# Performance work log

Measured on AMD Instinct MI355X. Metric: run time of the kernel, lower is better.

Reference implementation:

```python
import jax, jax.numpy as jnp
import numpy as np

B, H, W = 8, 64, 64
DIM1, DIM2 = 384, 256
NH, DH = 8, 32
INNER = NH * DH
EPS = 1e-5


def _layernorm(x, w, b):
    mu = jnp.mean(x, axis=-1, keepdims=True)
    var = jnp.mean((x - mu) ** 2, axis=-1, keepdims=True)
    return (x - mu) * jax.lax.rsqrt(var + EPS) * w + b


def _axial_attn(q, k, v, scale):
    # q,k,v: [B,H,W,nh,dh]; row attention over H, col attention over W
    sh = jnp.einsum('biwnd,bjwnd->bwnij', q, k) * scale  # [B,W,nh,H,H]
    oh = jnp.einsum('bwnij,bjwnd->biwnd', jax.nn.softmax(sh, axis=-1), v)
    sw = jnp.einsum('bhind,bhjnd->bhnij', q, k) * scale  # [B,H,nh,W,W]
    ow = jnp.einsum('bhnij,bhjnd->bhind', jax.nn.softmax(sw, axis=-1), v)
    return oh + ow  # [B,H,W,nh,dh]


def setup_inputs() -> dict:
    key = jax.random.key(0)
    ks = jax.random.split(key, 16)
    s1 = 1.0 / np.sqrt(DIM1)
    s2 = 1.0 / np.sqrt(DIM2)
    si = 1.0 / np.sqrt(INNER)
    return {
        'x1': jax.random.normal(ks[0], (B, DIM1, H, W), jnp.float32),
        'x2': jax.random.normal(ks[1], (B, DIM2, H, W), jnp.float32),
        'ln1q_w': jnp.ones((DIM1,), jnp.float32),
        'ln1q_b': jnp.zeros((DIM1,), jnp.float32),
        'ln2kv_w': jnp.ones((DIM2,), jnp.float32),
        'ln2kv_b': jnp.zeros((DIM2,), jnp.float32),
        'Wq1': jax.random.normal(ks[2], (DIM1, INNER), jnp.float32) * s1,
        'Wkv2': jax.random.normal(ks[3], (DIM2, 2 * INNER), jnp.float32) * s2,
        'Wout1': jax.random.normal(ks[4], (INNER, DIM2), jnp.float32) * si,
        'bout1': jnp.zeros((DIM2,), jnp.float32),
        'ln2q_w': jnp.ones((DIM2,), jnp.float32),
        'ln2q_b': jnp.zeros((DIM2,), jnp.float32),
        'ln1kv_w': jnp.ones((DIM1,), jnp.float32),
        'ln1kv_b': jnp.zeros((DIM1,), jnp.float32),
        'Wq2': jax.random.normal(ks[5], (DIM2, INNER), jnp.float32) * s2,
        'Wkv1': jax.random.normal(ks[6], (DIM1, 2 * INNER), jnp.float32) * s1,
        'Wout2': jax.random.normal(ks[7], (INNER, DIM2), jnp.float32) * si,
        'bout2': jnp.zeros((DIM2,), jnp.float32),
        'Wsc': jax.random.normal(ks[8], (DIM2, DIM1), jnp.float32) * s1,  # 1x1 conv [out,in]
        'bn_gamma': jnp.ones((DIM2,), jnp.float32),
        'bn_beta': jnp.zeros((DIM2,), jnp.float32),
        'bn_mean': jnp.zeros((DIM2,), jnp.float32),
        'bn_var': jnp.ones((DIM2,), jnp.float32),
    }


def reference(x1, x2, ln1q_w, ln1q_b, ln2kv_w, ln2kv_b, Wq1, Wkv2, Wout1, bout1,
              ln2q_w, ln2q_b, ln1kv_w, ln1kv_b, Wq2, Wkv1, Wout2, bout2,
              Wsc, bn_gamma, bn_beta, bn_mean, bn_var):
    b, c1, h, w = x1.shape
    scale = DH ** -0.5
    x1f = jnp.transpose(x1, (0, 2, 3, 1))  # [B,H,W,C1]
    x2f = jnp.transpose(x2, (0, 2, 3, 1))  # [B,H,W,C2]

    def heads(t):
        return t.reshape(b, h, w, NH, DH)

    # branch 1: q from x1, kv from x2
    q1 = _layernorm(x1f, ln1q_w, ln1q_b) @ Wq1
    kv2 = _layernorm(x2f, ln2kv_w, ln2kv_b) @ Wkv2
    k2, v2 = jnp.split(kv2, 2, axis=-1)
    o1 = _axial_attn(heads(q1), heads(k2), heads(v2), scale)
    fused1 = o1.reshape(b, h, w, INNER) @ Wout1 + bout1
    # shortcut: 1x1 conv + BN (inference stats)
    sc = jnp.einsum('bhwc,oc->bhwo', x1f, Wsc)
    sc = (sc - bn_mean) * jax.lax.rsqrt(bn_var + EPS) * bn_gamma + bn_beta
    y1 = sc + fused1

    # branch 2: q from x2, kv from x1
    q2 = _layernorm(x2f, ln2q_w, ln2q_b) @ Wq2
    kv1 = _layernorm(x1f, ln1kv_w, ln1kv_b) @ Wkv1
    k1, v1 = jnp.split(kv1, 2, axis=-1)
    o2 = _axial_attn(heads(q2), heads(k1), heads(v1), scale)
    fused2 = o2.reshape(b, h, w, INNER) @ Wout2 + bout2
    y2 = x2f + fused2

    out = y1 + y2  # [B,H,W,C2]
    return jnp.transpose(out, (0, 3, 1, 2))
```

## Files before the change

### kernel.cpp

```cpp
#include <hip/hip_runtime.h>

typedef unsigned short u16;
typedef unsigned int u32;
typedef float v4f __attribute__((ext_vector_type(4)));
typedef __bf16 v8bf __attribute__((ext_vector_type(8)));

__device__ __forceinline__ float bf2f(u16 v) {
  union { u32 u; float f; } x; x.u = ((u32)v) << 16; return x.f;
}
__device__ __forceinline__ u16 f2bf(float f) {
  union { float f; u32 u; } x; x.f = f;
  u32 u = x.u;
  return (u16)((u + 0x7FFFu + ((u >> 16) & 1u)) >> 16);
}
__device__ __forceinline__ u32 f2u(float f) {
  union { float f; u32 u; } x; x.f = f; return x.u;
}
__device__ __forceinline__ u32 pk2bf(float a, float b) {
  const u32 au = f2u(a) + 0x8000u;
  const u32 bu = f2u(b) + 0x8000u;
  return (bu & 0xFFFF0000u) | (au >> 16);
}

struct Ptrs { const void* p[23]; };

__global__ __launch_bounds__(256) void convert_all(Ptrs ps, u16* __restrict__ cx1,
                                                   u16* __restrict__ cx2,
                                                   u16* __restrict__ cw) {
  static const int sz[23]  = {12582912, 8388608, 384, 384, 256, 256, 98304, 131072,
                              65536, 256, 256, 256, 384, 384, 65536, 196608, 65536,
                              256, 98304, 256, 256, 256, 256};
  static const int off[23] = {0, 0, 0, 384, 768, 1024, 1280, 99584, 230656, 296192,
                              296448, 296704, 296960, 297344, 297728, 363264, 559872,
                              625408, 625664, 723968, 724224, 724480, 724736};
  const int ti = blockIdx.y;
  const int n8 = sz[ti] >> 3;
  const bool isf32 = (((const u32*)ps.p[2])[0] == 0x3F800000u);
  u16* dst = (ti == 0) ? cx1 : (ti == 1) ? cx2 : (cw + off[ti]);
  const void* src = ps.p[ti];
  const int stride = gridDim.x * blockDim.x;
  for (int i = blockIdx.x * blockDim.x + threadIdx.x; i < n8; i += stride) {
    if (isf32) {
      const float4 f0 = ((const float4*)src)[2*i];
      const float4 f1 = ((const float4*)src)[2*i + 1];
      u16 tmp[8];
      tmp[0] = f2bf(f0.x); tmp[1] = f2bf(f0.y); tmp[2] = f2bf(f0.z); tmp[3] = f2bf(f0.w);
      tmp[4] = f2bf(f1.x); tmp[5] = f2bf(f1.y); tmp[6] = f2bf(f1.z); tmp[7] = f2bf(f1.w);
      ((uint4*)dst)[i] = *(const uint4*)tmp;
    } else {
      ((uint4*)dst)[i] = ((const uint4*)src)[i];
    }
  }
}

__global__ void prep_bt(const u16* __restrict__ lnq_w, const u16* __restrict__ lnq_b,
                        const u16* __restrict__ lnkv_w, const u16* __restrict__ lnkv_b,
                        const u16* __restrict__ Wq, const u16* __restrict__ Wkv,
                        u16* __restrict__ BT, float* __restrict__ bias) {
  const int C = blockDim.x;
  const int j = blockIdx.x;
  const int c = threadIdx.x;
  float w, bco, wv;
  if (j < 256) { w = bf2f(lnq_w[c]); bco = bf2f(lnq_b[c]); wv = bf2f(Wq[c*256 + j]); }
  else         { w = bf2f(lnkv_w[c]); bco = bf2f(lnkv_b[c]); wv = bf2f(Wkv[c*512 + (j-256)]); }
  BT[(size_t)j*C + c] = f2bf(w * wv);
  __shared__ float red[384];
  red[c] = bco * wv;
  __syncthreads();
  if (c == 0) { float s = 0.f; for (int i = 0; i < C; i++) s += red[i]; bias[j] = s; }
}

__global__ void prep_fin(const u16* __restrict__ Wout1, const u16* __restrict__ Wout2,
                         const u16* __restrict__ Wsc, const u16* __restrict__ bout1,
                         const u16* __restrict__ bout2, const u16* __restrict__ gam,
                         const u16* __restrict__ bet, const u16* __restrict__ mean,
                         const u16* __restrict__ var, u16* __restrict__ BT,
                         float* __restrict__ bias) {
  const int o = blockIdx.x, t = threadIdx.x;
  const float g = rsqrtf(bf2f(var[o]) + 1e-5f) * bf2f(gam[o]);
  for (int idx = t; idx < 1408; idx += 256) {
    float v;
    if (idx < 512)       v = bf2f(Wout1[(idx & 255)*256 + o]);
    else if (idx < 1024) v = bf2f(Wout2[((idx - 512) & 255)*256 + o]);
    else                 v = bf2f(Wsc[o*384 + (idx - 1024)]) * g;
    BT[(size_t)o*1408 + idx] = f2bf(v);
  }
  if (t == 0) bias[o] = bf2f(bet[o]) - bf2f(mean[o])*g + bf2f(bout1[o]) + bf2f(bout2[o]);
}

__global__ __launch_bounds__(256) void ln_c384(const u16* __restrict__ x,
                                               u16* __restrict__ xn, u16* __restrict__ xraw) {
  __shared__ u16 tile[384*66];
  __shared__ float rsum[4][64], rsq[4][64], smean[64], srstd[64];
  const int t = threadIdx.x, w = t & 63, g = t >> 6;
  const int bh = blockIdx.x, b = bh >> 6, h = bh & 63;
  const u16* src = x + (size_t)b*384*4096 + h*64 + w;
  float sum = 0.f, sq = 0.f;
  for (int j = 0; j < 96; j++) {
    const int c = g*96 + j;
    const u16 uv = src[(size_t)c*4096];
    tile[c*66 + w] = uv;
    const float v = bf2f(uv); sum += v; sq += v*v;
  }
  rsum[g][w] = sum; rsq[g][w] = sq;
  __syncthreads();
  if (t < 64) {
    const float s = rsum[0][t]+rsum[1][t]+rsum[2][t]+rsum[3][t];
    const float q = rsq[0][t]+rsq[1][t]+rsq[2][t]+rsq[3][t];
    const float mean = s * (1.0f/384.0f);
    float var = q * (1.0f/384.0f) - mean*mean;
    if (var < 0.f) var = 0.f;
    smean[t] = mean; srstd[t] = rsqrtf(var + 1e-5f);
  }
  __syncthreads();
  const size_t pos0 = (size_t)bh * 64;
  for (int i = 0; i < 96; i++) {
    const int flat = i*256 + t;
    const int ww = flat / 384, c = flat - ww*384;
    const u16 uv = tile[c*66 + ww];
    const float v = (bf2f(uv) - smean[ww]) * srstd[ww];
    const size_t p = pos0 + ww;
    xn[p*384 + c] = f2bf(v);
    xraw[p*384 + c] = uv;
  }
}

__global__ __launch_bounds__(256) void ln_c256(const u16* __restrict__ x,
                                               u16* __restrict__ xn) {
  __shared__ u16 tile[256*66];
  __shared__ float rsum[4][64], rsq[4][64], smean[64], srstd[64];
  const int t = threadIdx.x, w = t & 63, g = t >> 6;
  const int bh = blockIdx.x, b = bh >> 6, h = bh & 63;
  const u16* src = x + (size_t)b*256*4096 + h*64 + w;
  float sum = 0.f, sq = 0.f;
  for (int j = 0; j < 64; j++) {
    const int c = g*64 + j;
    const u16 uv = src[(size_t)c*4096];
    tile[c*66 + w] = uv;
    const float v = bf2f(uv); sum += v; sq += v*v;
  }
  rsum[g][w] = sum; rsq[g][w] = sq;
  __syncthreads();
  if (t < 64) {
    const float s = rsum[0][t]+rsum[1][t]+rsum[2][t]+rsum[3][t];
    const float q = rsq[0][t]+rsq[1][t]+rsq[2][t]+rsq[3][t];
    const float mean = s * (1.0f/256.0f);
    float var = q * (1.0f/256.0f) - mean*mean;
    if (var < 0.f) var = 0.f;
    smean[t] = mean; srstd[t] = rsqrtf(var + 1e-5f);
  }
  __syncthreads();
  const size_t pos0 = (size_t)bh * 64;
  for (int i = 0; i < 64; i++) {
    const int flat = i*256 + t;
    const int ww = flat >> 8, c = flat & 255;
    const float v = (bf2f(tile[c*66 + ww]) - smean[ww]) * srstd[ww];
    xn[(pos0 + ww)*256 + c] = f2bf(v);
  }
}

__global__ __launch_bounds__(256) void gemm_bt(const u16* __restrict__ A,
                                               const u16* __restrict__ BT,
                                               u16* __restrict__ C,
                                               const float* __restrict__ bias,
                                               int N, int K) {
  __shared__ u16 lsA[128*40];
  __shared__ u16 lsB[128*40];
  const int t = threadIdx.x;
  const int m0 = blockIdx.x * 128, n0 = blockIdx.y * 128;
  const int lane = t & 63, wv = t >> 6;
  const int wm = wv & 1, wn = wv >> 1;
  const int lo = lane & 15, hi = lane >> 4;
  const int r0 = t >> 2, c8 = (t & 3) << 3;
  const u16* Ab = A + (size_t)(m0 + r0) * K + c8;
  const u16* Bb = BT + (size_t)(n0 + r0) * K + c8;
  v4f acc[4][4] = {};
  for (int kb = 0; kb < K; kb += 32) {
    uint4 a0 = *(const uint4*)(Ab + kb);
    uint4 a1 = *(const uint4*)(Ab + (size_t)64*K + kb);
    uint4 b0 = *(const uint4*)(Bb + kb);
    uint4 b1 = *(const uint4*)(Bb + (size_t)64*K + kb);
    __syncthreads();
    *(uint4*)&lsA[r0*40 + c8] = a0;
    *(uint4*)&lsA[(r0+64)*40 + c8] = a1;
    *(uint4*)&lsB[r0*40 + c8] = b0;
    *(uint4*)&lsB[(r0+64)*40 + c8] = b1;
    __syncthreads();
    v8bf av[4], bv[4];
#pragma unroll
    for (int i = 0; i < 4; i++) av[i] = *(const v8bf*)&lsA[(wm*64 + i*16 + lo)*40 + hi*8];
#pragma unroll
    for (int i = 0; i < 4; i++) bv[i] = *(const v8bf*)&lsB[(wn*64 + i*16 + lo)*40 + hi*8];
#pragma unroll
    for (int mt = 0; mt < 4; mt++)
#pragma unroll
      for (int nt = 0; nt < 4; nt++)
        acc[mt][nt] = __builtin_amdgcn_mfma_f32_16x16x32_bf16(av[mt], bv[nt], acc[mt][nt], 0, 0, 0);
  }
#pragma unroll
  for (int mt = 0; mt < 4; mt++) {
    const int row = m0 + wm*64 + mt*16 + hi*4;
#pragma unroll
    for (int nt = 0; nt < 4; nt++) {
      const int col = n0 + wn*64 + nt*16 + lo;
      const float bs = bias[col];
#pragma unroll
      for (int r = 0; r < 4; r++)
        C[(size_t)(row + r) * N + col] = f2bf(acc[mt][nt][r] + bs);
    }
  }
}

__global__ __launch_bounds__(256) void gemm_final(const u16* __restrict__ Ao,
                                                  const u16* __restrict__ Ar,
                                                  const u16* __restrict__ BT,
                                                  const float* __restrict__ bias,
                                                  const u16* __restrict__ x2c,
                                                  const u32* __restrict__ probe,
                                                  void* __restrict__ outv) {
  __shared__ u16 smem[16640];
  u16* lsA = smem;
  u16* lsB = smem + 5120;
  const int t = threadIdx.x;
  const int m0 = blockIdx.x * 128, n0 = blockIdx.y * 128;
  const int lane = t & 63, wv = t >> 6;
  const int wm = wv & 1, wn = wv >> 1;
  const int lo = lane & 15, hi = lane >> 4;
  const int r0 = t >> 2, c8 = (t & 3) << 3;
  const u16* ArR = Ar + (size_t)(m0 + r0) * 384 + c8;
  const u16* Bb  = BT + (size_t)(n0 + r0) * 1408 + c8;
  v4f acc[4][4] = {};
  for (int kb = 0; kb < 1408; kb += 32) {
    uint4 a0, a1;
    if (kb < 1024) {
      const u16* ap = Ao + ((size_t)(kb >> 5) * 32768 + m0 + r0) * 32 + c8;
      a0 = *(const uint4*)ap;
      a1 = *(const uint4*)(ap + 64*32);
    } else {
      a0 = *(const uint4*)(ArR + (kb-1024));
      a1 = *(const uint4*)(ArR + 64*384 + (kb-1024));
    }
    uint4 b0 = *(const uint4*)(Bb + kb);
    uint4 b1 = *(const uint4*)(Bb + 64*1408 + kb);
    __syncthreads();
    *(uint4*)&lsA[r0*40 + c8] = a0;
    *(uint4*)&lsA[(r0+64)*40 + c8] = a1;
    *(uint4*)&lsB[r0*40 + c8] = b0;
    *(uint4*)&lsB[(r0+64)*40 + c8] = b1;
    __syncthreads();
    v8bf av[4], bv[4];
#pragma unroll
    for (int i = 0; i < 4; i++) av[i] = *(const v8bf*)&lsA[(wm*64 + i*16 + lo)*40 + hi*8];
#pragma unroll
    for (int i = 0; i < 4; i++) bv[i] = *(const v8bf*)&lsB[(wn*64 + i*16 + lo)*40 + hi*8];
#pragma unroll
    for (int mt = 0; mt < 4; mt++)
#pragma unroll
      for (int nt = 0; nt < 4; nt++)
        acc[mt][nt] = __builtin_amdgcn_mfma_f32_16x16x32_bf16(av[mt], bv[nt], acc[mt][nt], 0, 0, 0);
  }
  __syncthreads();
#pragma unroll
  for (int mt = 0; mt < 4; mt++)
#pragma unroll
    for (int nt = 0; nt < 4; nt++) {
      const int nl = wn*64 + nt*16 + lo;
      const float bs = bias[n0 + nl];
#pragma unroll
      for (int r = 0; r < 4; r++)
        smem[(wm*64 + mt*16 + hi*4 + r)*130 + nl] = f2bf(acc[mt][nt][r] + bs);
    }
  __syncthreads();
  const bool isf32 = (probe[0] == 0x3F800000u);
  const int bh0 = blockIdx.x * 2;
  for (int i = 0; i < 64; i++) {
    const int flat = i*256 + t;
    const int nl = flat >> 7;
    const int rem = flat & 127;
    const int mb = rem >> 6, w = rem & 63;
    const int bh = bh0 + mb, b = bh >> 6, h = bh & 63;
    const size_t oidx = ((size_t)(b*256 + n0 + nl)*64 + h)*64 + w;
    const float val = bf2f(smem[(mb*64 + w)*130 + nl]) + bf2f(x2c[oidx]);
    if (isf32) ((float*)outv)[oidx] = val;
    else       ((u16*)outv)[oidx]   = f2bf(val);
  }
}

__global__ __launch_bounds__(512) void attn(const u16* __restrict__ qkv1,
                                            const u16* __restrict__ qkv2,
                                            u16* __restrict__ Ao) {
  __shared__ __attribute__((aligned(16))) u16 smem[8 * 2560];
  const int t = threadIdx.x;
  const int head = t >> 6, lane = t & 63;
  const int lo = lane & 15, quad = lane >> 4;
  u16* sw = smem + head * 2560;
  const int bx = blockIdx.x;
  const int z = blockIdx.y;
  const int br = z >> 1, dir = z & 1;
  const int b = bx >> 6, x = bx & 63;
  const u16* Qb  = (br == 0) ? qkv1 : qkv2;
  const u16* KVb = (br == 0) ? qkv2 : qkv1;
  const int qc = head*32, kc = 256 + head*32, vc = 512 + head*32;
  const int pbase = (dir == 0) ? (b*4096 + x) : ((b*64 + x)*64);
  const int pstr  = (dir == 0) ? 64 : 1;

  {
    const u16* vr = KVb + (size_t)(pbase + lane*pstr)*768 + vc;
    u16 vbuf[32];
#pragma unroll
    for (int i = 0; i < 4; i++) *(uint4*)&vbuf[i*8] = *(const uint4*)(vr + i*8);
    const int khi = lane >> 3, klo = lane & 7;
#pragma unroll
    for (int d = 0; d < 32; d++)
      sw[d*64 + ((khi ^ (d & 7)) << 3) + klo] = vbuf[d];
  }
  __syncthreads();

  v8bf qa[4], ka[4];
#pragma unroll
  for (int i = 0; i < 4; i++) {
    const size_t p = (size_t)(pbase + (i*16 + lo)*pstr) * 768;
    qa[i] = *(const v8bf*)(Qb + p + qc + quad*8);
    ka[i] = *(const v8bf*)(KVb + p + kc + quad*8);
  }

  v4f s[4][4];
#pragma unroll
  for (int qt = 0; qt < 4; qt++)
#pragma unroll
    for (int kt = 0; kt < 4; kt++) {
      v4f z4 = {};
      s[qt][kt] = __builtin_amdgcn_mfma_f32_16x16x32_bf16(ka[kt], qa[qt], z4, 0, 0, 0);
    }

  v8bf va[2][2];
#pragma unroll
  for (int mt = 0; mt < 2; mt++)
#pragma unroll
    for (int ks = 0; ks < 2; ks++) {
      const int d = mt*16 + lo;
      va[mt][ks] = *(const v8bf*)&sw[d*64 + (((ks*4 + quad) ^ (d & 7)) << 3)];
    }

  const float scale = 0.17677669529663687f;
  v4f o[2][4] = {};
#pragma unroll
  for (int qt = 0; qt < 4; qt++) {
    float tv[16];
    float mx = -1e30f;
#pragma unroll
    for (int kt = 0; kt < 4; kt++)
#pragma unroll
      for (int r = 0; r < 4; r++) {
        const float v = s[qt][kt][r] * scale;
        tv[kt*4 + r] = v;
        mx = fmaxf(mx, v);
      }
    mx = fmaxf(mx, __shfl_xor(mx, 16));
    mx = fmaxf(mx, __shfl_xor(mx, 32));
    float sm = 0.f;
#pragma unroll
    for (int i = 0; i < 16; i++) { tv[i] = __expf(tv[i] - mx); sm += tv[i]; }
    sm += __shfl_xor(sm, 16);
    sm += __shfl_xor(sm, 32);
    const float inv = 1.0f / sm;
    u32 pk[4][2];
#pragma unroll
    for (int kt = 0; kt < 4; kt++)
#pragma unroll
      for (int rp = 0; rp < 2; rp++)
        pk[kt][rp] = pk2bf(tv[kt*4 + rp*2] * inv, tv[kt*4 + rp*2 + 1] * inv);
    u32 pw[2][4];
#pragma unroll
    for (int ks = 0; ks < 2; ks++)
#pragma unroll
      for (int rp = 0; rp < 2; rp++) {
        const u32 v16 = (quad < 2)  ? pk[2*ks][rp]   : pk[2*ks+1][rp];
        const u32 v32 = (quad < 2)  ? pk[2*ks+1][rp] : pk[2*ks][rp];
        const u32 v48 = (quad & 1)  ? pk[2*ks+1][rp] : pk[2*ks][rp];
        const u32 r16 = (u32)__shfl_xor((int)v16, 16);
        const u32 r32 = (u32)__shfl_xor((int)v32, 32);
        const u32 r48 = (u32)__shfl_xor((int)v48, 48);
        const u32 wlo = (quad == 0) ? pk[2*ks][rp] : (quad == 1) ? r48 : (quad == 2) ? r32 : r16;
        const u32 whi = (quad == 0) ? r16 : (quad == 1) ? r32 : (quad == 2) ? r48 : pk[2*ks+1][rp];
        pw[ks][rp] = wlo;
        pw[ks][2 + rp] = whi;
      }
#pragma unroll
    for (int ks = 0; ks < 2; ks++) {
      union { u32 u[4]; v8bf v; } pb;
      pb.u[0] = pw[ks][0]; pb.u[1] = pw[ks][1]; pb.u[2] = pw[ks][2]; pb.u[3] = pw[ks][3];
#pragma unroll
      for (int mt = 0; mt < 2; mt++)
        o[mt][qt] = __builtin_amdgcn_mfma_f32_16x16x32_bf16(va[mt][ks], pb.v, o[mt][qt], 0, 0, 0);
    }
  }

  __syncthreads();
#pragma unroll
  for (int mt = 0; mt < 2; mt++)
#pragma unroll
    for (int nt = 0; nt < 4; nt++)
#pragma unroll
      for (int rp = 0; rp < 2; rp++) {
        const u32 pkv = pk2bf(o[mt][nt][rp*2], o[mt][nt][rp*2 + 1]);
        *(u32*)&sw[(nt*16 + lo)*40 + mt*16 + quad*4 + rp*2] = pkv;
      }
  __syncthreads();
  {
    const size_t sbase = (size_t)(z*8 + head) * 32768 + pbase;
#pragma unroll
    for (int it = 0; it < 4; it++) {
      const int chunk = it*64 + lane;
      const int row = chunk >> 2, ic = chunk & 3;
      *(uint4*)&Ao[(sbase + (size_t)row*pstr)*32 + ic*8] = *(const uint4*)&sw[row*40 + ic*8];
    }
  }
}

extern "C" void kernel_launch(void* const* d_in, const int* in_sizes, int n_in,
                              void* d_out, int out_size, void* d_ws, size_t ws_size,
                              hipStream_t stream) {
  char* ws = (char*)d_ws;
  u16* Ao    = (u16*)(ws);
  u16* Araw  = (u16*)(ws + 67108864);
  u16* qkv1  = (u16*)(ws + 92274688);
  u16* qkv2  = (u16*)(ws + 142606336);
  u16* cx2   = (u16*)(ws + 192937984);
  u16* cw    = (u16*)(ws + 209715200);
  u16* BT1   = (u16*)(ws + 211165184);
  u16* BT2   = (u16*)(ws + 211755008);
  u16* BTf   = (u16*)(ws + 212148224);
  float* bias1 = (float*)(ws + 212869120);
  float* bias2 = (float*)(ws + 212872192);
  float* biasf = (float*)(ws + 212875264);
  u16* cx1 = qkv1;
  u16* x1n = Ao;
  u16* x2n = Ao + 12582912;

  u16* c_ln1q_w = cw + 0,     *c_ln1q_b = cw + 384;
  u16* c_ln2kv_w = cw + 768,  *c_ln2kv_b = cw + 1024;
  u16* c_Wq1 = cw + 1280,     *c_Wkv2 = cw + 99584;
  u16* c_Wout1 = cw + 230656, *c_bout1 = cw + 296192;
  u16* c_ln2q_w = cw + 296448,*c_ln2q_b = cw + 296704;
  u16* c_ln1kv_w = cw + 296960,*c_ln1kv_b = cw + 297344;
  u16* c_Wq2 = cw + 297728,   *c_Wkv1 = cw + 363264;
  u16* c_Wout2 = cw + 559872, *c_bout2 = cw + 625408;
  u16* c_Wsc = cw + 625664;
  u16* c_bn_g = cw + 723968,  *c_bn_b = cw + 724224;
  u16* c_bn_m = cw + 724480,  *c_bn_v = cw + 724736;

  Ptrs ps;
  for (int i = 0; i < 23; i++) ps.p[i] = d_in[i];

  convert_all<<<dim3(512, 23), 256, 0, stream>>>(ps, cx1, cx2, cw);
  prep_bt<<<768, 384, 0, stream>>>(c_ln1q_w, c_ln1q_b, c_ln1kv_w, c_ln1kv_b, c_Wq1, c_Wkv1, BT1, bias1);
  prep_bt<<<768, 256, 0, stream>>>(c_ln2q_w, c_ln2q_b, c_ln2kv_w, c_ln2kv_b, c_Wq2, c_Wkv2, BT2, bias2);
  prep_fin<<<256, 256, 0, stream>>>(c_Wout1, c_Wout2, c_Wsc, c_bout1, c_bout2,
                                    c_bn_g, c_bn_b, c_bn_m, c_bn_v, BTf, biasf);
  ln_c384<<<512, 256, 0, stream>>>(cx1, x1n, Araw);
  ln_c256<<<512, 256, 0, stream>>>(cx2, x2n);
  gemm_bt<<<dim3(256, 6), 256, 0, stream>>>(x1n, BT1, qkv1, bias1, 768, 384);
  gemm_bt<<<dim3(256, 6), 256, 0, stream>>>(x2n, BT2, qkv2, bias2, 768, 256);
  attn<<<dim3(512, 4), 512, 0, stream>>>(qkv1, qkv2, Ao);
  gemm_final<<<dim3(256, 2), 256, 0, stream>>>(Ao, Araw, BTf, biasf, cx2,
                                               (const u32*)d_in[2], d_out);
}
```

Baseline: 371.1 us.

## Prefetch next K-tile into registers in GEMMs; widen final GEMM to 512 threads

```diff
diff --git a/kernel.cpp b/kernel.cpp
--- a/kernel.cpp
+++ b/kernel.cpp
@@ -174,18 +174,24 @@
   const int r0 = t >> 2, c8 = (t & 3) << 3;
   const u16* Ab = A + (size_t)(m0 + r0) * K + c8;
   const u16* Bb = BT + (size_t)(n0 + r0) * K + c8;
+  uint4 a0 = *(const uint4*)(Ab);
+  uint4 a1 = *(const uint4*)(Ab + (size_t)64*K);
+  uint4 b0 = *(const uint4*)(Bb);
+  uint4 b1 = *(const uint4*)(Bb + (size_t)64*K);
   v4f acc[4][4] = {};
   for (int kb = 0; kb < K; kb += 32) {
-    uint4 a0 = *(const uint4*)(Ab + kb);
-    uint4 a1 = *(const uint4*)(Ab + (size_t)64*K + kb);
-    uint4 b0 = *(const uint4*)(Bb + kb);
-    uint4 b1 = *(const uint4*)(Bb + (size_t)64*K + kb);
     __syncthreads();
     *(uint4*)&lsA[r0*40 + c8] = a0;
     *(uint4*)&lsA[(r0+64)*40 + c8] = a1;
     *(uint4*)&lsB[r0*40 + c8] = b0;
     *(uint4*)&lsB[(r0+64)*40 + c8] = b1;
     __syncthreads();
+    if (kb + 32 < K) {
+      a0 = *(const uint4*)(Ab + kb + 32);
+      a1 = *(const uint4*)(Ab + (size_t)64*K + kb + 32);
+      b0 = *(const uint4*)(Bb + kb + 32);
+      b1 = *(const uint4*)(Bb + (size_t)64*K + kb + 32);
+    }
     v8bf av[4], bv[4];
 #pragma unroll
     for (int i = 0; i < 4; i++) av[i] = *(const v8bf*)&lsA[(wm*64 + i*16 + lo)*40 + hi*8];
@@ -211,7 +217,7 @@
   }
 }
 
-__global__ __launch_bounds__(256) void gemm_final(const u16* __restrict__ Ao,
+__global__ __launch_bounds__(512) void gemm_final(const u16* __restrict__ Ao,
                                                   const u16* __restrict__ Ar,
                                                   const u16* __restrict__ BT,
                                                   const float* __restrict__ bias,
@@ -224,57 +230,56 @@
   const int t = threadIdx.x;
   const int m0 = blockIdx.x * 128, n0 = blockIdx.y * 128;
   const int lane = t & 63, wv = t >> 6;
-  const int wm = wv & 1, wn = wv >> 1;
+  const int wm = wv >> 1, wn = wv & 1;
   const int lo = lane & 15, hi = lane >> 4;
   const int r0 = t >> 2, c8 = (t & 3) << 3;
   const u16* ArR = Ar + (size_t)(m0 + r0) * 384 + c8;
   const u16* Bb  = BT + (size_t)(n0 + r0) * 1408 + c8;
-  v4f acc[4][4] = {};
+
+  uint4 a, bq;
+  {
+    a = *(const uint4*)(Ao + ((size_t)(0) * 32768 + m0 + r0) * 32 + c8);
+    bq = *(const uint4*)(Bb);
+  }
+  v4f acc[2][4] = {};
   for (int kb = 0; kb < 1408; kb += 32) {
-    uint4 a0, a1;
-    if (kb < 1024) {
-      const u16* ap = Ao + ((size_t)(kb >> 5) * 32768 + m0 + r0) * 32 + c8;
-      a0 = *(const uint4*)ap;
-      a1 = *(const uint4*)(ap + 64*32);
-    } else {
-      a0 = *(const uint4*)(ArR + (kb-1024));
-      a1 = *(const uint4*)(ArR + 64*384 + (kb-1024));
-    }
-    uint4 b0 = *(const uint4*)(Bb + kb);
-    uint4 b1 = *(const uint4*)(Bb + 64*1408 + kb);
     __syncthreads();
-    *(uint4*)&lsA[r0*40 + c8] = a0;
-    *(uint4*)&lsA[(r0+64)*40 + c8] = a1;
-    *(uint4*)&lsB[r0*40 + c8] = b0;
-    *(uint4*)&lsB[(r0+64)*40 + c8] = b1;
+    *(uint4*)&lsA[r0*40 + c8] = a;
+    *(uint4*)&lsB[r0*40 + c8] = bq;
     __syncthreads();
-    v8bf av[4], bv[4];
-#pragma unroll
-    for (int i = 0; i < 4; i++) av[i] = *(const v8bf*)&lsA[(wm*64 + i*16 + lo)*40 + hi*8];
+    const int kn = kb + 32;
+    if (kn < 1408) {
+      if (kn < 1024) a = *(const uint4*)(Ao + ((size_t)(kn >> 5) * 32768 + m0 + r0) * 32 + c8);
+      else           a = *(const uint4*)(ArR + (kn - 1024));
+      bq = *(const uint4*)(Bb + kn);
+    }
+    v8bf av[2], bv[4];
+#pragma unroll
+    for (int i = 0; i < 2; i++) av[i] = *(const v8bf*)&lsA[(wm*32 + i*16 + lo)*40 + hi*8];
 #pragma unroll
     for (int i = 0; i < 4; i++) bv[i] = *(const v8bf*)&lsB[(wn*64 + i*16 + lo)*40 + hi*8];
 #pragma unroll
-    for (int mt = 0; mt < 4; mt++)
+    for (int mt = 0; mt < 2; mt++)
 #pragma unroll
       for (int nt = 0; nt < 4; nt++)
         acc[mt][nt] = __builtin_amdgcn_mfma_f32_16x16x32_bf16(av[mt], bv[nt], acc[mt][nt], 0, 0, 0);
   }
   __syncthreads();
 #pragma unroll
-  for (int mt = 0; mt < 4; mt++)
+  for (int mt = 0; mt < 2; mt++)
 #pragma unroll
     for (int nt = 0; nt < 4; nt++) {
       const int nl = wn*64 + nt*16 + lo;
       const float bs = bias[n0 + nl];
 #pragma unroll
       for (int r = 0; r < 4; r++)
-        smem[(wm*64 + mt*16 + hi*4 + r)*130 + nl] = f2bf(acc[mt][nt][r] + bs);
+        smem[(wm*32 + mt*16 + hi*4 + r)*130 + nl] = f2bf(acc[mt][nt][r] + bs);
     }
   __syncthreads();
   const bool isf32 = (probe[0] == 0x3F800000u);
   const int bh0 = blockIdx.x * 2;
-  for (int i = 0; i < 64; i++) {
-    const int flat = i*256 + t;
+  for (int i = 0; i < 32; i++) {
+    const int flat = i*512 + t;
     const int nl = flat >> 7;
     const int rem = flat & 127;
     const int mb = rem >> 6, w = rem & 63;
@@ -463,6 +468,6 @@
   gemm_bt<<<dim3(256, 6), 256, 0, stream>>>(x1n, BT1, qkv1, bias1, 768, 384);
   gemm_bt<<<dim3(256, 6), 256, 0, stream>>>(x2n, BT2, qkv2, bias2, 768, 256);
   attn<<<dim3(512, 4), 512, 0, stream>>>(qkv1, qkv2, Ao);
-  gemm_final<<<dim3(256, 2), 256, 0, stream>>>(Ao, Araw, BTf, biasf, cx2,
+  gemm_final<<<dim3(256, 2), 512, 0, stream>>>(Ao, Araw, BTf, biasf, cx2,
                                                (const u32*)d_in[2], d_out);
 }
```

Result: faster. 358.9 us (-3.3%).
